# Kernel optimization log

Measured on AMD Instinct MI355X. Metric: run time of the kernel, lower is better.

The kernel has to match this reference:

```python
import jax, jax.numpy as jnp
import numpy as np

N_AC, N_W, D_IN = 40000, 20000, 128
H, DH, D_OUT = 4, 64, 64
E_TIC, E_W, E_REL = 400000, 200000, 400000
NEG = 0.2  # DGL GATConv leaky_relu negative slope


def _edge_softmax(e, dst, n_dst):
    # e: (E, H) edge logits; softmax over edges sharing the same dst node
    m = jax.ops.segment_max(e, dst, num_segments=n_dst)
    m = jnp.where(jnp.isfinite(m), m, 0.0)
    ex = jnp.exp(e - m[dst])
    s = jax.ops.segment_sum(ex, dst, num_segments=n_dst)
    return ex / (s[dst] + 1e-9)


def _gat(x_src, x_dst, src, dst, ew, W, al, ar, b, n_dst, act):
    # DGL GATConv (eval mode: dropouts are identity). al/ar: (H, D)
    Hh, Dd = al.shape
    z_src = (x_src @ W).reshape(-1, Hh, Dd)
    z_dst = (x_dst @ W).reshape(-1, Hh, Dd)
    el = jnp.einsum('nhd,hd->nh', z_src, al)
    er = jnp.einsum('nhd,hd->nh', z_dst, ar)
    e = jax.nn.leaky_relu(el[src] + er[dst], NEG)              # (E, H)
    a = _edge_softmax(e, dst, n_dst) * ew[:, None]             # attention * edge_weight
    out = jax.ops.segment_sum(z_src[src] * a[:, :, None], dst, num_segments=n_dst)
    out = out + b.reshape(1, Hh, Dd)
    return act(out) if act is not None else out


def _forward(x_ac, x_w, w_tic, w_w, w_rel,
             W1_tic, al1_tic, ar1_tic, b1_tic,
             W1_w, al1_w, ar1_w, b1_w,
             W1_rel, al1_rel, ar1_rel, b1_rel,
             W2_tic, al2_tic, ar2_tic, b2_tic,
             W2_w, al2_w, ar2_w, b2_w,
             W2_rel, al2_rel, ar2_rel, b2_rel,
             src_tic, dst_tic, src_w, dst_w, src_rel, dst_rel):
    elu = jax.nn.elu
    # --- layer 1 (H=4 heads, ELU activation inside GATConv) ---
    h_tic = _gat(x_ac, x_ac, src_tic, dst_tic, w_tic, W1_tic, al1_tic, ar1_tic, b1_tic, N_AC, elu)
    h_w1 = _gat(x_w, x_w, src_w, dst_w, w_w, W1_w, al1_w, ar1_w, b1_w, N_W, elu)
    h_rel = _gat(x_ac, x_w, src_rel, dst_rel, w_rel, W1_rel, al1_rel, ar1_rel, b1_rel, N_W, elu)
    # HeteroGraphConv aggregate='mean' over etypes per dst node type, flatten heads, ReLU
    h_ac = jax.nn.relu(h_tic.reshape(N_AC, -1))
    h_word = jax.nn.relu(((h_w1 + h_rel) * 0.5).reshape(N_W, -1))
    # --- layer 2 (single head, no activation) ---
    o_tic = _gat(h_ac, h_ac, src_tic, dst_tic, w_tic, W2_tic, al2_tic, ar2_tic, b2_tic, N_AC, None)
    o_w = _gat(h_word, h_word, src_w, dst_w, w_w, W2_w, al2_w, ar2_w, b2_w, N_W, None)
    o_rel = _gat(h_ac, h_word, src_rel, dst_rel, w_rel, W2_rel, al2_rel, ar2_rel, b2_rel, N_W, None)
    return (o_tic.reshape(N_AC, -1), ((o_w + o_rel) * 0.5).reshape(N_W, -1))


def setup_inputs() -> dict:
    key = jax.random.key(0)
    ks = iter(jax.random.split(key, 48))
    def p(shape):
        return jax.random.normal(next(ks), shape, jnp.float32) * 0.05
    inp = {
        'x_ac': jax.random.normal(next(ks), (N_AC, D_IN), jnp.float32),
        'x_w': jax.random.normal(next(ks), (N_W, D_IN), jnp.float32),
        'w_tic': jax.random.uniform(next(ks), (E_TIC,), jnp.float32),
        'w_w': jax.random.uniform(next(ks), (E_W,), jnp.float32),
        'w_rel': jax.random.uniform(next(ks), (E_REL,), jnp.float32),
    }
    # per-etype GATConv params: layer1 (H heads), layer2 (1 head)
    for name, fin, h, d in [('1_tic', D_IN, H, DH), ('1_w', D_IN, H, DH), ('1_rel', D_IN, H, DH),
                            ('2_tic', H * DH, 1, D_OUT), ('2_w', H * DH, 1, D_OUT), ('2_rel', H * DH, 1, D_OUT)]:
        inp['W' + name] = p((fin, h * d))
        inp['al' + name] = p((h, d))
        inp['ar' + name] = p((h, d))
        inp['b' + name] = p((h * d,))
    inp['src_tic'] = jax.random.randint(next(ks), (E_TIC,), 0, N_AC, jnp.int32)
    inp['dst_tic'] = jax.random.randint(next(ks), (E_TIC,), 0, N_AC, jnp.int32)
    inp['src_w'] = jax.random.randint(next(ks), (E_W,), 0, N_W, jnp.int32)
    inp['dst_w'] = jax.random.randint(next(ks), (E_W,), 0, N_W, jnp.int32)
    inp['src_rel'] = jax.random.randint(next(ks), (E_REL,), 0, N_AC, jnp.int32)
    inp['dst_rel'] = jax.random.randint(next(ks), (E_REL,), 0, N_W, jnp.int32)
    return inp


def reference(x_ac, x_w, w_tic, w_w, w_rel,
              W1_tic, al1_tic, ar1_tic, b1_tic,
              W1_w, al1_w, ar1_w, b1_w,
              W1_rel, al1_rel, ar1_rel, b1_rel,
              W2_tic, al2_tic, ar2_tic, b2_tic,
              W2_w, al2_w, ar2_w, b2_w,
              W2_rel, al2_rel, ar2_rel, b2_rel,
              src_tic, dst_tic, src_w, dst_w, src_rel, dst_rel):
    return _forward(x_ac, x_w, w_tic, w_w, w_rel,
                    W1_tic, al1_tic, ar1_tic, b1_tic,
                    W1_w, al1_w, ar1_w, b1_w,
                    W1_rel, al1_rel, ar1_rel, b1_rel,
                    W2_tic, al2_tic, ar2_tic, b2_tic,
                    W2_w, al2_w, ar2_w, b2_w,
                    W2_rel, al2_rel, ar2_rel, b2_rel,
                    src_tic, dst_tic, src_w, dst_w, src_rel, dst_rel)
```

## Files before the change

kernel.cpp:

```cpp
#include <hip/hip_runtime.h>
#include <hip/hip_bf16.h>

typedef unsigned short ushort_t;
typedef __attribute__((ext_vector_type(8))) short bf16x8;
typedef __attribute__((ext_vector_type(4))) float f32x4;

#define N_AC 40000
#define N_W  20000
#define D_IN 128
#define NH   4
#define HD   256
#define DOUT 64
#define E_TIC 400000
#define E_W   200000
#define E_REL 400000
#define E_ALL 1000000
#define N_ALL 80000
#define NEG 0.2f
#define CAP 96
#define FCH 4096
#define ELLW 64

__device__ __forceinline__ float bf2f(ushort_t u) {
    return __uint_as_float(((unsigned int)u) << 16);
}
__device__ __forceinline__ ushort_t f2bf(float v) {
    unsigned u = __float_as_uint(v);
    unsigned r = (u + 0x7fffu + ((u >> 16) & 1u)) >> 16;
    return (ushort_t)r;
}
__device__ __forceinline__ float ldf(const void* p, size_t i, int f) {
    return f ? ((const float*)p)[i] : bf2f(((const ushort_t*)p)[i]);
}
__device__ __forceinline__ float lrelu_exp(float v) {
    v = v > 0.f ? v : NEG * v;
    return __expf(v);
}

__global__ void detect_dtype(const ushort_t* __restrict__ x, int* __restrict__ flag) {
    __shared__ int hit;
    if (threadIdx.x == 0) hit = 0;
    __syncthreads();
    for (int i = threadIdx.x; i < 4096; i += 256) {
        float v = bf2f(x[i]);
        if (!(fabsf(v) <= 1e4f)) atomicOr(&hit, 1);
    }
    __syncthreads();
    if (threadIdx.x == 0) flag[0] = hit ? 1 : 0;
}

struct CvtTab { const void* src[24]; int n[24]; int off[24]; };
__global__ __launch_bounds__(256) void cvt_inputs(CvtTab t, float* __restrict__ par,
                                                  const int* __restrict__ flagp) {
    int ent = blockIdx.x >> 3, sub = blockIdx.x & 7;
    int f = flagp[0];
    const void* s = t.src[ent];
    int n = t.n[ent];
    float* d = par + t.off[ent];
    for (int i = sub * 256 + threadIdx.x; i < n; i += 8 * 256)
        d[i] = f ? ((const float*)s)[i] : bf2f(((const ushort_t*)s)[i]);
}

struct QTab { int woff[2]; int aoff[2]; int qoff[2]; int K[2]; int Hh[2]; };
__global__ __launch_bounds__(256) void make_q(QTab t, float* __restrict__ par) {
    int b = blockIdx.x;
    int k = threadIdx.x;
    int K = t.K[b], Hh = t.Hh[b];
    if (k >= K) return;
    const float* W = par + t.woff[b];
    const float* a = par + t.aoff[b];
    float* q = par + t.qoff[b];
    int HDc = Hh * 64;
    for (int h = 0; h < Hh; ++h) {
        float s = 0.f;
        for (int d = 0; d < 64; ++d) s += W[(size_t)k * HDc + h * 64 + d] * a[h * 64 + d];
        q[k * Hh + h] = s;
    }
}

struct PTab { int woff[6]; int toff[6]; int Klog[6]; int N[6]; };
__global__ __launch_bounds__(256) void pack_wt(PTab t, const float* __restrict__ par,
                                               ushort_t* __restrict__ wt) {
    int m = blockIdx.x >> 4, sub = blockIdx.x & 15;
    int Klog = t.Klog[m], K = 1 << Klog, Nn = t.N[m];
    int tot = K * Nn;
    const float* Wp = par + t.woff[m];
    ushort_t* d = wt + t.toff[m];
    for (int i = sub * 256 + threadIdx.x; i < tot; i += 16 * 256) {
        int n = i >> Klog, k = i & (K - 1);
        d[i] = f2bf(Wp[(size_t)k * Nn + n]);
    }
}


__device__ __forceinline__ void dev_mgemm1(int b, const void* X, int f,
                                           const ushort_t* WT, ushort_t* Zb,
                                           const float* alp, const float* arp,
                                           float* elo, float* ero) {
    const int w = threadIdx.x >> 6, l = threadIdx.x & 63;
    const int row0 = b * 16;
    const int lr = l & 15, lk = l >> 4;

    bf16x8 a[4];
    if (!f) {
        const ushort_t* xp = (const ushort_t*)X + (size_t)(row0 + lr) * 128 + lk * 8;
        #pragma unroll
        for (int ks = 0; ks < 4; ++ks) a[ks] = *(const bf16x8*)(xp + ks * 32);
    } else {
        const float* xp = (const float*)X + (size_t)(row0 + lr) * 128 + lk * 8;
        #pragma unroll
        for (int ks = 0; ks < 4; ++ks)
            #pragma unroll
            for (int j = 0; j < 8; ++j) a[ks][j] = (short)f2bf(xp[ks * 32 + j]);
    }

    f32x4 acc[4] = {{0.f,0.f,0.f,0.f},{0.f,0.f,0.f,0.f},{0.f,0.f,0.f,0.f},{0.f,0.f,0.f,0.f}};
    const int col0 = w * 64;
    #pragma unroll
    for (int ks = 0; ks < 4; ++ks) {
        #pragma unroll
        for (int nt = 0; nt < 4; ++nt) {
            bf16x8 bb = *(const bf16x8*)(WT + (size_t)(col0 + nt * 16 + lr) * 128 + ks * 32 + lk * 8);
            acc[nt] = __builtin_amdgcn_mfma_f32_16x16x32_bf16(a[ks], bb, acc[nt], 0, 0, 0);
        }
    }
    #pragma unroll
    for (int nt = 0; nt < 4; ++nt)
        #pragma unroll
        for (int r = 0; r < 4; ++r)
            Zb[(size_t)(row0 + lk * 4 + r) * HD + col0 + nt * 16 + lr] = f2bf(acc[nt][r]);

    if (alp) {
        float a0 = alp[col0 + lr], a1 = alp[col0 + 16 + lr],
              a2 = alp[col0 + 32 + lr], a3 = alp[col0 + 48 + lr];
        #pragma unroll
        for (int r = 0; r < 4; ++r) {
            float v = acc[0][r] * a0 + acc[1][r] * a1 + acc[2][r] * a2 + acc[3][r] * a3;
            v += __shfl_xor(v, 1, 64); v += __shfl_xor(v, 2, 64);
            v += __shfl_xor(v, 4, 64); v += __shfl_xor(v, 8, 64);
            if (lr == r) elo[(size_t)(row0 + lk * 4 + r) * 4 + w] = v;
        }
    }
    if (arp) {
        float a0 = arp[col0 + lr], a1 = arp[col0 + 16 + lr],
              a2 = arp[col0 + 32 + lr], a3 = arp[col0 + 48 + lr];
        #pragma unroll
        for (int r = 0; r < 4; ++r) {
            float v = acc[0][r] * a0 + acc[1][r] * a1 + acc[2][r] * a2 + acc[3][r] * a3;
            v += __shfl_xor(v, 1, 64); v += __shfl_xor(v, 2, 64);
            v += __shfl_xor(v, 4, 64); v += __shfl_xor(v, 8, 64);
            if (lr == r) ero[(size_t)(row0 + lk * 4 + r) * 4 + w] = v;
        }
    }
}

__device__ __forceinline__ void dev_fill_ell1(int b,
        const int* s0, const int* d0, const void* w0,
        const int* s1, const int* d1, const void* w1,
        const int* s2, const int* d2, const void* w2,
        int f, int* cnt, unsigned* adj) {
    int e = b * 256 + threadIdx.x;
    if (e >= E_ALL) return;
    int g, sn; float ew;
    if (e < E_TIC) {
        g = d0[e]; sn = s0[e]; ew = ldf(w0, e, f);
    } else if (e < E_TIC + E_W) {
        int le = e - E_TIC;
        g = N_AC + d1[le]; sn = s1[le]; ew = ldf(w1, le, f);
    } else {
        int le = e - E_TIC - E_W;
        g = N_AC + N_W + d2[le]; sn = s2[le]; ew = ldf(w2, le, f);
    }
    int r = atomicAdd(&cnt[g], 1);
    if (r < ELLW)
        adj[(size_t)g * ELLW + r] = (unsigned)(sn & 0xFFFF) | ((unsigned)f2bf(ew) << 16);
}

__device__ __forceinline__ void dev_elr1(int b, const void* X, int f,
                                         const float* q0, float* o0,
                                         int N, int D, int Hh) {
    __shared__ float qs[512];
    const int tid = threadIdx.x;
    const int tot = D * Hh;
    for (int i = tid; i < tot; i += 256) {
        int k, h;
        if (Hh == 4) { k = i >> 2; h = i & 3; } else { k = i; h = 0; }
        qs[h * D + k] = q0[i];
    }
    __syncthreads();
    const int wid = tid >> 6, lane = tid & 63;
    const int n = b * 4 + wid;
    if (n >= N) return;
    const int J = D >> 6;
    float x[4];
    for (int j = 0; j < J; ++j) x[j] = ldf(X, (size_t)n * D + j * 64 + lane, f);
    for (int h = 0; h < Hh; ++h) {
        float v = 0.f;
        for (int j = 0; j < J; ++j) v += x[j] * qs[h * D + j * 64 + lane];
        #pragma unroll
        for (int o = 32; o > 0; o >>= 1) v += __shfl_down(v, o, 64);
        if (lane == 0) o0[n * Hh + h] = v;
    }
}

template <int MODE>
__device__ __forceinline__ void dev_gat1(int b,
        const int* rp, const int* degp, int gbase, int ell,
        const unsigned* adj, const ushort_t* zb,
        const float* el, const float* er, const float* bias,
        ushort_t* H, int N, const float* q2, float* e2out) {
    __shared__ float atl[4][CAP * 4];
    __shared__ int   snl[4][CAP];
    const int w = threadIdx.x >> 6, lane = threadIdx.x & 63;
    const int n = b * 4 + w;
    if (n >= N) return;
    const int h = lane >> 4;
    int beg, deg;
    if (ell) {
        int g = gbase + n;
        beg = g * ELLW;
        deg = degp[g];
        deg = deg < ELLW ? deg : ELLW;
    } else {
        beg = rp[n];
        deg = rp[n + 1] - beg;
    }
    const float4* el4 = (const float4*)el;
    const float4 ern = ((const float4*)er)[n];

    float4 ss = make_float4(0.f, 0.f, 0.f, 0.f);
    for (int base = 0; base < deg; base += 64) {
        int i = base + lane;
        if (i < deg) {
            unsigned ae = adj[beg + i];
            int sn = ae & 0xFFFF;
            float4 e = el4[sn];
            float x0 = lrelu_exp(e.x + ern.x);
            float x1 = lrelu_exp(e.y + ern.y);
            float x2 = lrelu_exp(e.z + ern.z);
            float x3 = lrelu_exp(e.w + ern.w);
            ss.x += x0; ss.y += x1; ss.z += x2; ss.w += x3;
            if (i < CAP) {
                float ew = bf2f((ushort_t)(ae >> 16));
                float4* dst4 = (float4*)&atl[w][i * 4];
                *dst4 = make_float4(x0 * ew, x1 * ew, x2 * ew, x3 * ew);
                snl[w][i] = sn;
            }
        }
    }
    #pragma unroll
    for (int o = 32; o > 0; o >>= 1) {
        ss.x += __shfl_xor(ss.x, o, 64);
        ss.y += __shfl_xor(ss.y, o, 64);
        ss.z += __shfl_xor(ss.z, o, 64);
        ss.w += __shfl_xor(ss.w, o, 64);
    }
    const float sh = (h == 0) ? ss.x : (h == 1) ? ss.y : (h == 2) ? ss.z : ss.w;
    const float inv = 1.f / (sh + 1e-9f);
    const float erh = (h == 0) ? ern.x : (h == 1) ? ern.y : (h == 2) ? ern.z : ern.w;

    float a0 = 0.f, a1 = 0.f, a2 = 0.f, a3 = 0.f;
    #pragma unroll 4
    for (int i = 0; i < deg; ++i) {
        int sn; float atv;
        if (i < CAP) {
            sn = snl[w][i];
            atv = atl[w][i * 4 + h];
        } else {
            unsigned ae = adj[beg + i];
            sn = ae & 0xFFFF;
            atv = lrelu_exp(el[sn * 4 + h] + erh) * bf2f((ushort_t)(ae >> 16));
        }
        ushort4 zv = *(const ushort4*)(zb + (size_t)sn * HD + lane * 4);
        a0 += bf2f(zv.x) * atv; a1 += bf2f(zv.y) * atv;
        a2 += bf2f(zv.z) * atv; a3 += bf2f(zv.w) * atv;
    }
    float4 bb = *(const float4*)(bias + lane * 4);
    a0 = a0 * inv + bb.x; a1 = a1 * inv + bb.y;
    a2 = a2 * inv + bb.z; a3 = a3 * inv + bb.w;

    ushort_t* hp = H + (size_t)n * HD + lane * 4;
    ushort4 o;
    if (MODE == 0) {
        o.x = f2bf(a0 > 0.f ? a0 : 0.f); o.y = f2bf(a1 > 0.f ? a1 : 0.f);
        o.z = f2bf(a2 > 0.f ? a2 : 0.f); o.w = f2bf(a3 > 0.f ? a3 : 0.f);
    } else if (MODE == 1) {
        o.x = f2bf(a0 > 0.f ? a0 : expm1f(a0)); o.y = f2bf(a1 > 0.f ? a1 : expm1f(a1));
        o.z = f2bf(a2 > 0.f ? a2 : expm1f(a2)); o.w = f2bf(a3 > 0.f ? a3 : expm1f(a3));
    } else {
        ushort4 hw = *(const ushort4*)hp;
        float v0 = (bf2f(hw.x) + (a0 > 0.f ? a0 : expm1f(a0))) * 0.5f;
        float v1 = (bf2f(hw.y) + (a1 > 0.f ? a1 : expm1f(a1))) * 0.5f;
        float v2 = (bf2f(hw.z) + (a2 > 0.f ? a2 : expm1f(a2))) * 0.5f;
        float v3 = (bf2f(hw.w) + (a3 > 0.f ? a3 : expm1f(a3))) * 0.5f;
        v0 = v0 > 0.f ? v0 : 0.f; v1 = v1 > 0.f ? v1 : 0.f;
        v2 = v2 > 0.f ? v2 : 0.f; v3 = v3 > 0.f ? v3 : 0.f;
        o.x = f2bf(v0); o.y = f2bf(v1); o.z = f2bf(v2); o.w = f2bf(v3);
        if (q2) {
            const int c4 = lane * 4;
            float d = v0 * q2[c4] + v1 * q2[c4 + 1] + v2 * q2[c4 + 2] + v3 * q2[c4 + 3];
            #pragma unroll
            for (int oo = 32; oo > 0; oo >>= 1) d += __shfl_xor(d, oo, 64);
            if (lane == 0) e2out[n] = d;
        }
    }
    *(ushort4*)hp = o;
}

struct FA {
    const int *s0, *d0; const void* w0;
    const int *s1, *d1; const void* w1;
    const int *s2, *d2; const void* w2;
    const int* flagp; int* cnt; unsigned* adj;
    const void* x_ac; const void* x_w;
    const ushort_t *WTt, *WTw, *WTr;
    ushort_t *Zt, *Zw, *Zr;
    const float *al1t, *ar1t, *al1w, *ar1w, *al1r;
    float *ELt, *ERt, *ELw, *ERw, *ELr, *ERr;
    const float* qer1r;
    unsigned c0, c1, c2, c3;
};
__global__ __launch_bounds__(256) void fused_a(FA a) {
    const unsigned b = blockIdx.x;
    const int f = a.flagp[0];
    if (b < a.c0) {
        dev_fill_ell1(b, a.s0, a.d0, a.w0, a.s1, a.d1, a.w1, a.s2, a.d2, a.w2,
                      f, a.cnt, a.adj);
    } else if (b < a.c1) {
        dev_mgemm1(b - a.c0, a.x_ac, f, a.WTt, a.Zt, a.al1t, a.ar1t, a.ELt, a.ERt);
    } else if (b < a.c2) {
        dev_mgemm1(b - a.c1, a.x_w, f, a.WTw, a.Zw, a.al1w, a.ar1w, a.ELw, a.ERw);
    } else if (b < a.c3) {
        dev_mgemm1(b - a.c2, a.x_ac, f, a.WTr, a.Zr, a.al1r, nullptr, a.ELr, nullptr);
    } else {
        dev_elr1(b - a.c3, a.x_w, f, a.qer1r, a.ERr, N_W, 128, 4);
    }
}

struct GT {
    const int* degp; const unsigned* adj;
    const ushort_t *Zt, *Zw;
    const float *ELt, *ERt, *ELw, *ERw, *b1t, *b1w;
    ushort_t *Hac, *Hw;
    unsigned b1;
};
__global__ __launch_bounds__(256) void gat1_tw(GT t) {
    if (blockIdx.x < t.b1)
        dev_gat1<0>(blockIdx.x, nullptr, t.degp, 0, 1, t.adj, t.Zt,
                    t.ELt, t.ERt, t.b1t, t.Hac, N_AC, nullptr, nullptr);
    else
        dev_gat1<1>(blockIdx.x - t.b1, nullptr, t.degp, N_AC, 1, t.adj, t.Zw,
                    t.ELw, t.ERw, t.b1w, t.Hw, N_W, nullptr, nullptr);
}

template <int MODE>
__global__ __launch_bounds__(256) void gat1(const int* __restrict__ rp,
                                            const int* __restrict__ degp,
                                            int gbase, int ell,
                                            const unsigned* __restrict__ adj,
                                            const ushort_t* __restrict__ zb,
                                            const float* __restrict__ el,
                                            const float* __restrict__ er,
                                            const float* __restrict__ bias,
                                            ushort_t* __restrict__ H, int N,
                                            const float* __restrict__ q2,
                                            float* __restrict__ e2out) {
    dev_gat1<MODE>(blockIdx.x, rp, degp, gbase, ell, adj, zb, el, er, bias, H, N, q2, e2out);
}

__global__ __launch_bounds__(256) void count3(const int* __restrict__ d0,
                                              const int* __restrict__ d1,
                                              const int* __restrict__ d2,
                                              int* __restrict__ cnt,
                                              int* __restrict__ rank) {
    int e = blockIdx.x * 256 + threadIdx.x;
    if (e >= E_ALL) return;
    int g;
    if (e < E_TIC) g = d0[e];
    else if (e < E_TIC + E_W) g = N_AC + d1[e - E_TIC];
    else g = N_AC + N_W + d2[e - E_TIC - E_W];
    rank[e] = atomicAdd(&cnt[g], 1);
}

__global__ __launch_bounds__(256) void scan_bsum(const int* __restrict__ cnt,
                                                 int* __restrict__ bsum, int N) {
    __shared__ int red[256];
    int i = blockIdx.x * 256 + threadIdx.x;
    red[threadIdx.x] = (i < N) ? cnt[i] : 0;
    __syncthreads();
    #pragma unroll
    for (int o = 128; o > 0; o >>= 1) {
        if (threadIdx.x < o) red[threadIdx.x] += red[threadIdx.x + o];
        __syncthreads();
    }
    if (threadIdx.x == 0) bsum[blockIdx.x] = red[0];
}

__global__ __launch_bounds__(512) void scan_top(int* __restrict__ bsum, int B) {
    __shared__ int sc[512];
    const int t = threadIdx.x;
    int v = (t < B) ? bsum[t] : 0;
    sc[t] = v;
    __syncthreads();
    #pragma unroll
    for (int o = 1; o < 512; o <<= 1) {
        int u = (t >= o) ? sc[t - o] : 0;
        __syncthreads();
        sc[t] += u;
        __syncthreads();
    }
    if (t < B) bsum[t] = sc[t] - v;
}

__global__ __launch_bounds__(256) void scan_out(const int* __restrict__ cnt,
                                                const int* __restrict__ bsum,
                                                int* __restrict__ rowptr, int N) {
    __shared__ int sc[256];
    const int t = threadIdx.x;
    int i = blockIdx.x * 256 + t;
    int v = (i < N) ? cnt[i] : 0;
    sc[t] = v;
    __syncthreads();
    #pragma unroll
    for (int o = 1; o < 256; o <<= 1) {
        int u = (t >= o) ? sc[t - o] : 0;
        __syncthreads();
        sc[t] += u;
        __syncthreads();
    }
    int ex = sc[t] - v + bsum[blockIdx.x];
    if (i < N) {
        rowptr[i] = ex;
        if (i == N - 1) rowptr[N] = ex + v;
    }
}

__global__ __launch_bounds__(256) void fill3(const int* __restrict__ s0, const int* __restrict__ d0, const void* __restrict__ w0,
                                             const int* __restrict__ s1, const int* __restrict__ d1, const void* __restrict__ w1,
                                             const int* __restrict__ s2, const int* __restrict__ d2, const void* __restrict__ w2,
                                             const int* __restrict__ flagp,
                                             const int* __restrict__ rp,
                                             const int* __restrict__ rank,
                                             unsigned* __restrict__ adj) {
    const int CB[9] = {0, 12500, 25000, 37500, 50000, 61250, 67500, 73750, 80000};
    const int cls = blockIdx.x & 7;
    const int lo = CB[cls], hi = CB[cls + 1];
    const int f = flagp[0];
    const int e0 = (blockIdx.x >> 3) * FCH;
    for (int i = threadIdx.x; i < FCH; i += 256) {
        int e = e0 + i;
        if (e >= E_ALL) return;
        int g;
        if (e < E_TIC) g = d0[e];
        else if (e < E_TIC + E_W) g = N_AC + d1[e - E_TIC];
        else g = N_AC + N_W + d2[e - E_TIC - E_W];
        if (g < lo || g >= hi) continue;
        int sn; float ew;
        if (e < E_TIC) { sn = s0[e]; ew = ldf(w0, e, f); }
        else if (e < E_TIC + E_W) { int le = e - E_TIC; sn = s1[le]; ew = ldf(w1, le, f); }
        else { int le = e - E_TIC - E_W; sn = s2[le]; ew = ldf(w2, le, f); }
        int pos = rp[g] + rank[e];
        adj[pos] = (unsigned)(sn & 0xFFFF) | ((unsigned)f2bf(ew) << 16);
    }
}

__global__ __launch_bounds__(256) void mgemm1(const void* __restrict__ X,
                                              const int* __restrict__ flagp,
                                              const ushort_t* __restrict__ WT,
                                              ushort_t* __restrict__ Zb,
                                              const float* __restrict__ alp,
                                              const float* __restrict__ arp,
                                              float* __restrict__ elo,
                                              float* __restrict__ ero) {
    dev_mgemm1(blockIdx.x, X, flagp[0], WT, Zb, alp, arp, elo, ero);
}

__global__ __launch_bounds__(256) void elr1(const void* __restrict__ X,
                                            const int* __restrict__ flagp,
                                            const float* __restrict__ q0,
                                            float* __restrict__ o0,
                                            int N, int D, int Hh) {
    dev_elr1(blockIdx.x, X, flagp ? flagp[0] : 0, q0, o0, N, D, Hh);
}

struct G2 {
    const ushort_t* Hb[3]; const ushort_t* WT[3]; ushort_t* Zc[3];
    const float* al[3]; const float* ar[3]; float* el[3]; float* er[3];
    int N[3]; int b1, b2;
};
__global__ __launch_bounds__(256) void mgemm2_all(G2 t) {
    int s, b;
    if (blockIdx.x < (unsigned)t.b1) { s = 0; b = blockIdx.x; }
    else if (blockIdx.x < (unsigned)t.b2) { s = 1; b = blockIdx.x - t.b1; }
    else { s = 2; b = blockIdx.x - t.b2; }
    const int w = threadIdx.x >> 6, l = threadIdx.x & 63;
    const int row0 = b * 64 + w * 16;
    if (row0 >= t.N[s]) return;
    const int lr = l & 15, lk = l >> 4;
    const ushort_t* ap = t.Hb[s] + (size_t)(row0 + lr) * 256 + lk * 8;
    const ushort_t* WT = t.WT[s];

    f32x4 acc[4] = {{0.f,0.f,0.f,0.f},{0.f,0.f,0.f,0.f},{0.f,0.f,0.f,0.f},{0.f,0.f,0.f,0.f}};
    #pragma unroll
    for (int ks = 0; ks < 8; ++ks) {
        bf16x8 a = *(const bf16x8*)(ap + ks * 32);
        #pragma unroll
        for (int nt = 0; nt < 4; ++nt) {
            bf16x8 bb = *(const bf16x8*)(WT + (size_t)(nt * 16 + lr) * 256 + ks * 32 + lk * 8);
            acc[nt] = __builtin_amdgcn_mfma_f32_16x16x32_bf16(a, bb, acc[nt], 0, 0, 0);
        }
    }
    ushort_t* Zc = t.Zc[s];
    #pragma unroll
    for (int nt = 0; nt < 4; ++nt)
        #pragma unroll
        for (int r = 0; r < 4; ++r)
            Zc[(size_t)(row0 + lk * 4 + r) * DOUT + nt * 16 + lr] = f2bf(acc[nt][r]);

    if (t.al[s]) {
        const float* alp = t.al[s];
        float a0 = alp[lr], a1 = alp[16 + lr], a2 = alp[32 + lr], a3 = alp[48 + lr];
        #pragma unroll
        for (int r = 0; r < 4; ++r) {
            float v = acc[0][r] * a0 + acc[1][r] * a1 + acc[2][r] * a2 + acc[3][r] * a3;
            v += __shfl_xor(v, 1, 64); v += __shfl_xor(v, 2, 64);
            v += __shfl_xor(v, 4, 64); v += __shfl_xor(v, 8, 64);
            if (lr == r) t.el[s][row0 + lk * 4 + r] = v;
        }
    }
    if (t.ar[s]) {
        const float* arp = t.ar[s];
        float a0 = arp[lr], a1 = arp[16 + lr], a2 = arp[32 + lr], a3 = arp[48 + lr];
        #pragma unroll
        for (int r = 0; r < 4; ++r) {
            float v = acc[0][r] * a0 + acc[1][r] * a1 + acc[2][r] * a2 + acc[3][r] * a3;
            v += __shfl_xor(v, 1, 64); v += __shfl_xor(v, 2, 64);
            v += __shfl_xor(v, 4, 64); v += __shfl_xor(v, 8, 64);
            if (lr == r) t.er[s][row0 + lk * 4 + r] = v;
        }
    }
}

struct GA2 {
    const int* rp[3]; const int* degp; int gbase[3]; int ell;
    const ushort_t* zc[3]; const float* el[3]; const float* er[3];
    int N[3]; int b1, b2;
};
__global__ __launch_bounds__(256) void gat2_all(GA2 t, const unsigned* __restrict__ adj,
                                                const float* __restrict__ b2t,
                                                float* __restrict__ ACCw,
                                                float* __restrict__ ACCr,
                                                void* __restrict__ out,
                                                const int* __restrict__ flagp) {
    __shared__ float atl[4][CAP];
    __shared__ int   snl[4][CAP];
    int s, b;
    if (blockIdx.x < (unsigned)t.b1) { s = 0; b = blockIdx.x; }
    else if (blockIdx.x < (unsigned)t.b2) { s = 1; b = blockIdx.x - t.b1; }
    else { s = 2; b = blockIdx.x - t.b2; }
    const int w = threadIdx.x >> 6, lane = threadIdx.x & 63;
    const int n = b * 4 + w;
    if (n >= t.N[s]) return;
    const float* el = t.el[s];
    const ushort_t* zb = t.zc[s];
    int beg, deg;
    if (t.ell) {
        int g = t.gbase[s] + n;
        beg = g * ELLW;
        deg = t.degp[g];
        deg = deg < ELLW ? deg : ELLW;
    } else {
        const int* rp = t.rp[s];
        beg = rp[n];
        deg = rp[n + 1] - beg;
    }
    const float ern = t.er[s][n];

    float ssum = 0.f;
    for (int base = 0; base < deg; base += 64) {
        int i = base + lane;
        if (i < deg) {
            unsigned ae = adj[beg + i];
            int sn = ae & 0xFFFF;
            float x = lrelu_exp(el[sn] + ern);
            ssum += x;
            if (i < CAP) {
                atl[w][i] = x * bf2f((ushort_t)(ae >> 16));
                snl[w][i] = sn;
            }
        }
    }
    #pragma unroll
    for (int o = 32; o > 0; o >>= 1) ssum += __shfl_xor(ssum, o, 64);
    const float inv = 1.f / (ssum + 1e-9f);

    const int eoff = lane >> 4;
    const int c4 = (lane & 15) * 4;
    const int degc = deg < CAP ? deg : CAP;
    float a0 = 0.f, a1 = 0.f, a2 = 0.f, a3 = 0.f;
    #pragma unroll 2
    for (int i = 0; i < degc; i += 4) {
        int ii = i + eoff;
        int iic = ii < degc ? ii : degc - 1;
        float atv = ii < degc ? atl[w][iic] : 0.f;
        int sn = snl[w][iic];
        ushort4 zv = *(const ushort4*)(zb + (size_t)sn * DOUT + c4);
        a0 += bf2f(zv.x) * atv; a1 += bf2f(zv.y) * atv;
        a2 += bf2f(zv.z) * atv; a3 += bf2f(zv.w) * atv;
    }
    for (int i = CAP; i < deg; i += 4) {
        int ii = i + eoff;
        int iic = ii < deg ? ii : deg - 1;
        unsigned ae = adj[beg + iic];
        int sn = ae & 0xFFFF;
        float atv = lrelu_exp(el[sn] + ern) * bf2f((ushort_t)(ae >> 16));
        if (ii >= deg) atv = 0.f;
        ushort4 zv = *(const ushort4*)(zb + (size_t)sn * DOUT + c4);
        a0 += bf2f(zv.x) * atv; a1 += bf2f(zv.y) * atv;
        a2 += bf2f(zv.z) * atv; a3 += bf2f(zv.w) * atv;
    }
    a0 += __shfl_xor(a0, 16, 64); a0 += __shfl_xor(a0, 32, 64);
    a1 += __shfl_xor(a1, 16, 64); a1 += __shfl_xor(a1, 32, 64);
    a2 += __shfl_xor(a2, 16, 64); a2 += __shfl_xor(a2, 32, 64);
    a3 += __shfl_xor(a3, 16, 64); a3 += __shfl_xor(a3, 32, 64);
    a0 *= inv; a1 *= inv; a2 *= inv; a3 *= inv;

    if (lane < 16) {
        size_t o = (size_t)n * DOUT + c4;
        if (s == 0) {
            float v0 = a0 + b2t[c4], v1 = a1 + b2t[c4 + 1];
            float v2 = a2 + b2t[c4 + 2], v3 = a3 + b2t[c4 + 3];
            if (flagp[0]) { *(float4*)((float*)out + o) = make_float4(v0, v1, v2, v3); }
            else {
                ushort4 ov;
                ov.x = f2bf(v0); ov.y = f2bf(v1); ov.z = f2bf(v2); ov.w = f2bf(v3);
                *(ushort4*)((ushort_t*)out + o) = ov;
            }
        } else if (s == 1) {
            *(float4*)(ACCw + o) = make_float4(a0, a1, a2, a3);
        } else {
            *(float4*)(ACCr + o) = make_float4(a0, a1, a2, a3);
        }
    }
}

__global__ __launch_bounds__(256) void out_word(const float* __restrict__ aw,
                                                const float* __restrict__ bw,
                                                const float* __restrict__ ar_,
                                                const float* __restrict__ br,
                                                void* __restrict__ out,
                                                const int* __restrict__ flagp, int total) {
    int i = blockIdx.x * 256 + threadIdx.x;
    if (i >= total) return;
    int c = i & 63;
    float v = ((aw[i] + bw[c]) + (ar_[i] + br[c])) * 0.5f;
    size_t o = (size_t)N_AC * DOUT + i;
    if (flagp[0]) ((float*)out)[o] = v;
    else ((ushort_t*)out)[o] = f2bf(v);
}

extern "C" void kernel_launch(void* const* d_in, const int* in_sizes, int n_in,
                              void* d_out, int out_size, void* d_ws, size_t ws_size,
                              hipStream_t stream) {
    (void)in_sizes; (void)n_in; (void)out_size;

    const void* x_ac = d_in[0];
    const void* x_w  = d_in[1];
    const void* ew_tic = d_in[2];
    const void* ew_w   = d_in[3];
    const void* ew_rel = d_in[4];
    const int* src_tic = (const int*)d_in[29];
    const int* dst_tic = (const int*)d_in[30];
    const int* src_w   = (const int*)d_in[31];
    const int* dst_w   = (const int*)d_in[32];
    const int* src_rel = (const int*)d_in[33];
    const int* dst_rel = (const int*)d_in[34];

    float* ws = (float*)d_ws;
    int* FLAG = (int*)ws;

    float* PAR = ws + 16;
    const int o_W1t = 1000000, o_W1w = 1032768, o_W1r = 1065536;
    const int o_W2t = 1098304, o_W2w = 1114688, o_W2r = 1131072;
    const int o_al1t = 1147456, o_ar1t = 1147712, o_al1w = 1147968, o_ar1w = 1148224,
              o_al1r = 1148480, o_ar1r = 1148736;
    const int o_b1t = 1148992, o_b1w = 1149248, o_b1r = 1149504;
    const int o_al2t = 1149760, o_ar2t = 1149824, o_al2w = 1149888, o_ar2w = 1149952,
              o_al2r = 1150016, o_ar2r = 1150080;
    const int o_b2t = 1150144, o_b2w = 1150208, o_b2r = 1150272;
    const int o_qer1r = 1150400, o_qer2r = 1150912;

    float* EB   = ws + 1160016;
    float* ELt  = EB;
    float* ERt  = EB + 160000;
    float* ELw  = EB + 320000;
    float* ERw  = EB + 400000;
    float* ELr  = EB + 480000;
    float* ERr  = EB + 640000;
    float* E2tl = EB + 720000;
    float* E2tr = EB + 760000;
    float* E2wl = EB + 800000;
    float* E2wr = EB + 820000;
    float* E2rl = EB + 840000;
    float* E2rr = EB + 880000;

    const size_t NEED_A = 27813744ull * 4ull;
    const bool pathA = ws_size >= NEED_A;

    detect_dtype<<<1, 256, 0, stream>>>((const ushort_t*)x_ac, FLAG);

    CvtTab ct;
    const int srcIdx[24] = {5,6,7,8, 9,10,11,12, 13,14,15,16,
                            17,18,19,20, 21,22,23,24, 25,26,27,28};
    const int sizes[24] = {32768,256,256,256, 32768,256,256,256, 32768,256,256,256,
                           16384,64,64,64, 16384,64,64,64, 16384,64,64,64};
    const int offs[24] = {o_W1t,o_al1t,o_ar1t,o_b1t, o_W1w,o_al1w,o_ar1w,o_b1w,
                          o_W1r,o_al1r,o_ar1r,o_b1r,
                          o_W2t,o_al2t,o_ar2t,o_b2t, o_W2w,o_al2w,o_ar2w,o_b2w,
                          o_W2r,o_al2r,o_ar2r,o_b2r};
    for (int i = 0; i < 24; ++i) { ct.src[i] = d_in[srcIdx[i]]; ct.n[i] = sizes[i]; ct.off[i] = offs[i]; }
    cvt_inputs<<<24 * 8, 256, 0, stream>>>(ct, PAR, FLAG);

    QTab qt;
    qt.woff[0] = o_W1r; qt.aoff[0] = o_ar1r; qt.qoff[0] = o_qer1r; qt.K[0] = 128; qt.Hh[0] = 4;
    qt.woff[1] = o_W2r; qt.aoff[1] = o_ar2r; qt.qoff[1] = o_qer2r; qt.K[1] = 256; qt.Hh[1] = 1;
    make_q<<<2, 256, 0, stream>>>(qt, PAR);

    if (pathA) {
        ushort_t* Z_tic = (ushort_t*)(ws + 2060016);
        ushort_t* Z_w   = (ushort_t*)(ws + 7180016);
        ushort_t* Z_rel = (ushort_t*)(ws + 9740016);
        float* ACCw = ws + 9740016;
        float* ACCr = ws + 11020016;
        ushort_t* Hac = (ushort_t*)(ws + 14860016);
        ushort_t* Hw  = (ushort_t*)(ws + 19980016);
        ushort_t* WT  = (ushort_t*)(ws + 22540016);
        int* cntA = (int*)(ws + 22613744);
        unsigned* adjA = (unsigned*)(ws + 22693744);
        ushort_t* Zc_tic = Z_tic;
        ushort_t* Zc_w   = Z_tic + 2560000;
        ushort_t* Zc_r   = Z_tic + 3840000;
        const int t_W1t = 0, t_W1w = 32768, t_W1r = 65536,
                  t_W2t = 98304, t_W2w = 114688, t_W2r = 131072;

        PTab pt;
        const int pw[6] = {o_W1t, o_W1w, o_W1r, o_W2t, o_W2w, o_W2r};
        const int ptf[6] = {t_W1t, t_W1w, t_W1r, t_W2t, t_W2w, t_W2r};
        for (int i = 0; i < 6; ++i) {
            pt.woff[i] = pw[i]; pt.toff[i] = ptf[i];
            pt.Klog[i] = (i < 3) ? 7 : 8; pt.N[i] = (i < 3) ? 256 : 64;
        }
        pack_wt<<<6 * 16, 256, 0, stream>>>(pt, PAR, WT);

        hipMemsetAsync(cntA, 0, N_ALL * 4, stream);

        FA fa;
        fa.s0 = src_tic; fa.d0 = dst_tic; fa.w0 = ew_tic;
        fa.s1 = src_w;   fa.d1 = dst_w;   fa.w1 = ew_w;
        fa.s2 = src_rel; fa.d2 = dst_rel; fa.w2 = ew_rel;
        fa.flagp = FLAG; fa.cnt = cntA; fa.adj = adjA;
        fa.x_ac = x_ac; fa.x_w = x_w;
        fa.WTt = WT + t_W1t; fa.WTw = WT + t_W1w; fa.WTr = WT + t_W1r;
        fa.Zt = Z_tic; fa.Zw = Z_w; fa.Zr = Z_rel;
        fa.al1t = PAR + o_al1t; fa.ar1t = PAR + o_ar1t;
        fa.al1w = PAR + o_al1w; fa.ar1w = PAR + o_ar1w;
        fa.al1r = PAR + o_al1r;
        fa.ELt = ELt; fa.ERt = ERt; fa.ELw = ELw; fa.ERw = ERw;
        fa.ELr = ELr; fa.ERr = ERr;
        fa.qer1r = PAR + o_qer1r;
        fa.c0 = (E_ALL + 255) / 256;
        fa.c1 = fa.c0 + N_AC / 16;
        fa.c2 = fa.c1 + N_W / 16;
        fa.c3 = fa.c2 + N_AC / 16;
        const unsigned ctot = fa.c3 + N_W / 4;
        fused_a<<<ctot, 256, 0, stream>>>(fa);

        GT gt;
        gt.degp = cntA; gt.adj = adjA;
        gt.Zt = Z_tic; gt.Zw = Z_w;
        gt.ELt = ELt; gt.ERt = ERt; gt.ELw = ELw; gt.ERw = ERw;
        gt.b1t = PAR + o_b1t; gt.b1w = PAR + o_b1w;
        gt.Hac = Hac; gt.Hw = Hw;
        gt.b1 = N_AC / 4;
        gat1_tw<<<N_AC / 4 + N_W / 4, 256, 0, stream>>>(gt);

        gat1<2><<<N_W / 4, 256, 0, stream>>>(nullptr, cntA, N_AC + N_W, 1, adjA, Z_rel,
                                             ELr, ERr, PAR + o_b1r, Hw, N_W,
                                             PAR + o_qer2r, E2rr);

        G2 g2;
        g2.Hb[0] = Hac; g2.Hb[1] = Hw; g2.Hb[2] = Hac;
        g2.WT[0] = WT + t_W2t; g2.WT[1] = WT + t_W2w; g2.WT[2] = WT + t_W2r;
        g2.Zc[0] = Zc_tic; g2.Zc[1] = Zc_w; g2.Zc[2] = Zc_r;
        g2.al[0] = PAR + o_al2t; g2.al[1] = PAR + o_al2w; g2.al[2] = PAR + o_al2r;
        g2.ar[0] = PAR + o_ar2t; g2.ar[1] = PAR + o_ar2w; g2.ar[2] = nullptr;
        g2.el[0] = E2tl; g2.el[1] = E2wl; g2.el[2] = E2rl;
        g2.er[0] = E2tr; g2.er[1] = E2wr; g2.er[2] = nullptr;
        g2.N[0] = N_AC; g2.N[1] = N_W; g2.N[2] = N_AC;
        const int nb0 = (N_AC + 63) / 64, nb1 = (N_W + 63) / 64, nb2 = (N_AC + 63) / 64;
        g2.b1 = nb0; g2.b2 = nb0 + nb1;
        mgemm2_all<<<nb0 + nb1 + nb2, 256, 0, stream>>>(g2);

        GA2 ga;
        ga.rp[0] = ga.rp[1] = ga.rp[2] = nullptr;
        ga.degp = cntA; ga.ell = 1;
        ga.gbase[0] = 0; ga.gbase[1] = N_AC; ga.gbase[2] = N_AC + N_W;
        ga.zc[0] = Zc_tic; ga.zc[1] = Zc_w; ga.zc[2] = Zc_r;
        ga.el[0] = E2tl; ga.el[1] = E2wl; ga.el[2] = E2rl;
        ga.er[0] = E2tr; ga.er[1] = E2wr; ga.er[2] = E2rr;
        ga.N[0] = N_AC; ga.N[1] = N_W; ga.N[2] = N_W;
        const int gb0 = N_AC / 4, gb1 = N_W / 4, gb2 = N_W / 4;
        ga.b1 = gb0; ga.b2 = gb0 + gb1;
        gat2_all<<<gb0 + gb1 + gb2, 256, 0, stream>>>(ga, adjA, PAR + o_b2t, ACCw, ACCr, d_out, FLAG);

        out_word<<<(N_W * DOUT) / 256, 256, 0, stream>>>(ACCw, PAR + o_b2w, ACCr, PAR + o_b2r,
                                                         d_out, FLAG, N_W * DOUT);
    } else {
        float* ACC = ws + 2060016;
        ushort_t* Zb  = (ushort_t*)(ws + 3340016);
        ushort_t* Hac = (ushort_t*)(ws + 8460016);
        ushort_t* Hw  = (ushort_t*)(ws + 13580016);
        ushort_t* WT  = (ushort_t*)(ws + 16140016);
        const int t_W1t = 0, t_W1w = 32768, t_W1r = 65536,
                  t_W2t = 98304, t_W2w = 114688, t_W2r = 131072;
        int* IB = (int*)(ws + 16213760);
        int* rp   = IB;
        int* cnt  = IB + 80064;
        int* bsum = IB + 160128;
        unsigned* adj = (unsigned*)(IB + 160704);
        int* rank = IB + 1160704;
        float* ACCr = ws + 18374464;
        ushort_t* Zc_tic = Zb;
        ushort_t* Zc_w   = Zb + 2560000;
        ushort_t* Zc_r   = Zb + 3840000;

        PTab pt;
        const int pw[6] = {o_W1t, o_W1w, o_W1r, o_W2t, o_W2w, o_W2r};
        const int ptf[6] = {t_W1t, t_W1w, t_W1r, t_W2t, t_W2w, t_W2r};
        for (int i = 0; i < 6; ++i) {
            pt.woff[i] = pw[i]; pt.toff[i] = ptf[i];
            pt.Klog[i] = (i < 3) ? 7 : 8; pt.N[i] = (i < 3) ? 256 : 64;
        }
        pack_wt<<<6 * 16, 256, 0, stream>>>(pt, PAR, WT);

        {
            const int B = (N_ALL + 255) / 256;
            hipMemsetAsync(cnt, 0, N_ALL * 4, stream);
            count3<<<(E_ALL + 255) / 256, 256, 0, stream>>>(dst_tic, dst_w, dst_rel, cnt, rank);
            scan_bsum<<<B, 256, 0, stream>>>(cnt, bsum, N_ALL);
            scan_top<<<1, 512, 0, stream>>>(bsum, B);
            scan_out<<<B, 256, 0, stream>>>(cnt, bsum, rp, N_ALL);
            fill3<<<8 * ((E_ALL + FCH - 1) / FCH), 256, 0, stream>>>(
                src_tic, dst_tic, ew_tic, src_w, dst_w, ew_w, src_rel, dst_rel, ew_rel,
                FLAG, rp, rank, adj);
        }
        const int* rp_tic = rp;
        const int* rp_w   = rp + N_AC;
        const int* rp_rel = rp + N_AC + N_W;

        elr1<<<N_W / 4, 256, 0, stream>>>(x_w, FLAG, PAR + o_qer1r, ERr, N_W, 128, 4);

        mgemm1<<<N_AC / 16, 256, 0, stream>>>(x_ac, FLAG, WT + t_W1t, Zb,
                                              PAR + o_al1t, PAR + o_ar1t, ELt, ERt);
        gat1<0><<<N_AC / 4, 256, 0, stream>>>(rp_tic, nullptr, 0, 0, adj, Zb,
                                              ELt, ERt, PAR + o_b1t, Hac, N_AC, nullptr, nullptr);

        mgemm1<<<N_W / 16, 256, 0, stream>>>(x_w, FLAG, WT + t_W1w, Zb,
                                             PAR + o_al1w, PAR + o_ar1w, ELw, ERw);
        gat1<1><<<N_W / 4, 256, 0, stream>>>(rp_w, nullptr, 0, 0, adj, Zb,
                                             ELw, ERw, PAR + o_b1w, Hw, N_W, nullptr, nullptr);

        mgemm1<<<N_AC / 16, 256, 0, stream>>>(x_ac, FLAG, WT + t_W1r, Zb,
                                              PAR + o_al1r, nullptr, ELr, nullptr);
        gat1<2><<<N_W / 4, 256, 0, stream>>>(rp_rel, nullptr, 0, 0, adj, Zb,
                                             ELr, ERr, PAR + o_b1r, Hw, N_W, nullptr, nullptr);

        elr1<<<N_W / 4, 256, 0, stream>>>(Hw, nullptr, PAR + o_qer2r, E2rr, N_W, 256, 1);

        G2 g2;
        g2.Hb[0] = Hac; g2.Hb[1] = Hw; g2.Hb[2] = Hac;
        g2.WT[0] = WT + t_W2t; g2.WT[1] = WT + t_W2w; g2.WT[2] = WT + t_W2r;
        g2.Zc[0] = Zc_tic; g2.Zc[1] = Zc_w; g2.Zc[2] = Zc_r;
        g2.al[0] = PAR + o_al2t; g2.al[1] = PAR + o_al2w; g2.al[2] = PAR + o_al2r;
        g2.ar[0] = PAR + o_ar2t; g2.ar[1] = PAR + o_ar2w; g2.ar[2] = nullptr;
        g2.el[0] = E2tl; g2.el[1] = E2wl; g2.el[2] = E2rl;
        g2.er[0] = E2tr; g2.er[1] = E2wr; g2.er[2] = nullptr;
        g2.N[0] = N_AC; g2.N[1] = N_W; g2.N[2] = N_AC;
        const int nb0 = (N_AC + 63) / 64, nb1 = (N_W + 63) / 64, nb2 = (N_AC + 63) / 64;
        g2.b1 = nb0; g2.b2 = nb0 + nb1;
        mgemm2_all<<<nb0 + nb1 + nb2, 256, 0, stream>>>(g2);

        GA2 ga;
        ga.rp[0] = rp_tic; ga.rp[1] = rp_w; ga.rp[2] = rp_rel;
        ga.degp = nullptr; ga.ell = 0;
        ga.gbase[0] = ga.gbase[1] = ga.gbase[2] = 0;
        ga.zc[0] = Zc_tic; ga.zc[1] = Zc_w; ga.zc[2] = Zc_r;
        ga.el[0] = E2tl; ga.el[1] = E2wl; ga.el[2] = E2rl;
        ga.er[0] = E2tr; ga.er[1] = E2wr; ga.er[2] = E2rr;
        ga.N[0] = N_AC; ga.N[1] = N_W; ga.N[2] = N_W;
        const int gb0 = N_AC / 4, gb1 = N_W / 4, gb2 = N_W / 4;
        ga.b1 = gb0; ga.b2 = gb0 + gb1;
        gat2_all<<<gb0 + gb1 + gb2, 256, 0, stream>>>(ga, adj, PAR + o_b2t, ACC, ACCr, d_out, FLAG);

        out_word<<<(N_W * DOUT) / 256, 256, 0, stream>>>(ACC, PAR + o_b2w, ACCr, PAR + o_b2r,
                                                         d_out, FLAG, N_W * DOUT);
    }
}
```

Before: 349.4 us.

## Partition ELL fill by destination range to localize atomics and adj writes

Each ELL-fill block now handles a 4096-edge chunk but only inserts edges whose destination node falls into one of 8 node-range classes, so each block's atomics and adjacency writes cover a narrow slice of memory. The intent is better L2 locality for the scattered atomicAdd on counts and the adj stores. The cost is that every edge's dst is read 8 times and far fewer threads run per edge. The fallback path also drops the separate layer-2 elr1 launch by passing the qer2r parameters into gat1<2>, as the main path already does.

Result: faster. 318.8 us (-8.8%).

```diff
diff --git a/kernel.cpp b/kernel.cpp
--- a/kernel.cpp
+++ b/kernel.cpp
@@ -154,26 +154,31 @@
     }
 }
 
-__device__ __forceinline__ void dev_fill_ell1(int b,
+__device__ __forceinline__ void dev_fill_ell(int b,
         const int* s0, const int* d0, const void* w0,
         const int* s1, const int* d1, const void* w1,
         const int* s2, const int* d2, const void* w2,
         int f, int* cnt, unsigned* adj) {
-    int e = b * 256 + threadIdx.x;
-    if (e >= E_ALL) return;
-    int g, sn; float ew;
-    if (e < E_TIC) {
-        g = d0[e]; sn = s0[e]; ew = ldf(w0, e, f);
-    } else if (e < E_TIC + E_W) {
-        int le = e - E_TIC;
-        g = N_AC + d1[le]; sn = s1[le]; ew = ldf(w1, le, f);
-    } else {
-        int le = e - E_TIC - E_W;
-        g = N_AC + N_W + d2[le]; sn = s2[le]; ew = ldf(w2, le, f);
-    }
-    int r = atomicAdd(&cnt[g], 1);
-    if (r < ELLW)
-        adj[(size_t)g * ELLW + r] = (unsigned)(sn & 0xFFFF) | ((unsigned)f2bf(ew) << 16);
+    const int CB[9] = {0, 12500, 25000, 37500, 50000, 61250, 67500, 73750, 80000};
+    const int cls = b & 7;
+    const int lo = CB[cls], hi = CB[cls + 1];
+    const int e0 = (b >> 3) * FCH;
+    for (int i = threadIdx.x; i < FCH; i += 256) {
+        int e = e0 + i;
+        if (e >= E_ALL) return;
+        int g;
+        if (e < E_TIC) g = d0[e];
+        else if (e < E_TIC + E_W) g = N_AC + d1[e - E_TIC];
+        else g = N_AC + N_W + d2[e - E_TIC - E_W];
+        if (g < lo || g >= hi) continue;
+        int sn; float ew;
+        if (e < E_TIC) { sn = s0[e]; ew = ldf(w0, e, f); }
+        else if (e < E_TIC + E_W) { int le = e - E_TIC; sn = s1[le]; ew = ldf(w1, le, f); }
+        else { int le = e - E_TIC - E_W; sn = s2[le]; ew = ldf(w2, le, f); }
+        int r = atomicAdd(&cnt[g], 1);
+        if (r < ELLW)
+            adj[(size_t)g * ELLW + r] = (unsigned)(sn & 0xFFFF) | ((unsigned)f2bf(ew) << 16);
+    }
 }
 
 __device__ __forceinline__ void dev_elr1(int b, const void* X, int f,
@@ -324,8 +329,8 @@
     const unsigned b = blockIdx.x;
     const int f = a.flagp[0];
     if (b < a.c0) {
-        dev_fill_ell1(b, a.s0, a.d0, a.w0, a.s1, a.d1, a.w1, a.s2, a.d2, a.w2,
-                      f, a.cnt, a.adj);
+        dev_fill_ell(b, a.s0, a.d0, a.w0, a.s1, a.d1, a.w1, a.s2, a.d2, a.w2,
+                     f, a.cnt, a.adj);
     } else if (b < a.c1) {
         dev_mgemm1(b - a.c0, a.x_ac, f, a.WTt, a.Zt, a.al1t, a.ar1t, a.ELt, a.ERt);
     } else if (b < a.c2) {
@@ -768,7 +773,7 @@
         fa.ELt = ELt; fa.ERt = ERt; fa.ELw = ELw; fa.ERw = ERw;
         fa.ELr = ELr; fa.ERr = ERr;
         fa.qer1r = PAR + o_qer1r;
-        fa.c0 = (E_ALL + 255) / 256;
+        fa.c0 = 8 * ((E_ALL + FCH - 1) / FCH);
         fa.c1 = fa.c0 + N_AC / 16;
         fa.c2 = fa.c1 + N_W / 16;
         fa.c3 = fa.c2 + N_AC / 16;
@@ -873,9 +878,8 @@
         mgemm1<<<N_AC / 16, 256, 0, stream>>>(x_ac, FLAG, WT + t_W1r, Zb,
                                               PAR + o_al1r, nullptr, ELr, nullptr);
         gat1<2><<<N_W / 4, 256, 0, stream>>>(rp_rel, nullptr, 0, 0, adj, Zb,
-                                             ELr, ERr, PAR + o_b1r, Hw, N_W, nullptr, nullptr);
-
-        elr1<<<N_W / 4, 256, 0, stream>>>(Hw, nullptr, PAR + o_qer2r, E2rr, N_W, 256, 1);
+                                             ELr, ERr, PAR + o_b1r, Hw, N_W,
+                                             PAR + o_qer2r, E2rr);
 
         G2 g2;
         g2.Hb[0] = Hac; g2.Hb[1] = Hw; g2.Hb[2] = Hac;
```
